# Kernel optimization log

Measured on AMD Instinct MI355X. Metric: run time of the kernel, lower is better.

The kernel has to match this reference:

```python
import jax, jax.numpy as jnp
import numpy as np

HID = 512; HH = HID // 2; INP = 1; OUT = 1
INH = int(HID * 0.3); EXC = HID - INH            # 153 / 359
N = 3 * HH + 2 * HID + INP                       # 1793 total units
ALM_EXC_START = 3 * HH + HID                      # start of ALM excitatory block
T_CONST = 0.1; SIGMA_REC = 0.01
B, T = 128, 300


def _np_masks():
    rng = np.random.default_rng(0)
    n_zeros = int(np.ceil(0.9 * HH))
    sparse = np.ones((HH, HH), np.float32)
    for c in range(HH):
        sparse[rng.permutation(HH)[:n_zeros], c] = 0.0
    alm2str = np.concatenate([np.ones((HH, EXC), np.float32), np.zeros((HH, INH), np.float32)], 1)
    thal2d1 = np.concatenate([np.ones((HH // 2, HID), np.float32), np.zeros((HH // 2, HID), np.float32)], 0)
    alm2d1 = 1.0 - thal2d1
    iti2d1 = np.concatenate([np.ones((HH // 2, INP), np.float32), np.zeros((HH // 2, INP), np.float32)], 0)
    alm_sign = np.concatenate([np.ones(EXC, np.float32), -np.ones(INH, np.float32)])  # alm2alm_D diagonal
    return sparse, alm2str, thal2d1, alm2d1, iti2d1, alm_sign

_SPARSE, _ALM2STR, _THAL2D1M, _ALM2D1M, _ITI2D1M, _ALMSIGN = [jnp.asarray(a) for a in _np_masks()]


def _clip(w):
    return jnp.clip(w, 1e-10, 1.0)               # F.hardtanh(w, 1e-10, 1)


def _build_W(d12d1_w, d12d2_w, d22d1_w, d22d2_w, d22stn_w, d12thal_w, stn2thal_w,
             thal2alm_w, alm2alm_w, thal2d1_w, thal2d2_w, alm2d1_w, alm2d2_w,
             inp_w_d1, inp_w_d2):
    z_ss = jnp.zeros((HH, HH)); z_sl = jnp.zeros((HH, HID))
    z_ls = jnp.zeros((HID, HH)); z_ll = jnp.zeros((HID, HID))
    z_si = jnp.zeros((HH, INP)); z_li = jnp.zeros((HID, INP))
    # striatal recurrence: sparse_mask * hardtanh(w) @ (-I)
    d12d1 = -(_SPARSE * _clip(d12d1_w)); d12d2 = -(_SPARSE * _clip(d12d2_w))
    d22d1 = -(_SPARSE * _clip(d22d1_w)); d22d2 = -(_SPARSE * _clip(d22d2_w))
    row_d1 = jnp.concatenate([d12d1, d22d1, z_ss, _THAL2D1M * _clip(thal2d1_w),
                              _ALM2D1M * _ALM2STR * _clip(alm2d1_w), _ITI2D1M * _clip(inp_w_d1)], 1)
    row_d2 = jnp.concatenate([d12d2, d22d2, z_ss, _clip(thal2d2_w),
                              _ALM2STR * _clip(alm2d2_w), _clip(inp_w_d2)], 1)
    row_stn = jnp.concatenate([z_ss, _clip(d22stn_w), z_ss, z_sl, z_sl, z_si], 1)
    row_thal = jnp.concatenate([_clip(d12thal_w), z_ls, -_clip(stn2thal_w), z_ll, z_ll, z_li], 1)  # stn2thal @ (-I)
    row_alm = jnp.concatenate([z_ls, z_ls, z_ls, _clip(thal2alm_w),
                               _clip(alm2alm_w) * _ALMSIGN[None, :], z_li], 1)      # alm2alm @ D (Dale)
    row_iti = jnp.zeros((INP, N))
    return jnp.concatenate([row_d1, row_d2, row_stn, row_thal, row_alm, row_iti], 0)


def setup_inputs() -> dict:
    key = jax.random.key(0)
    ks = jax.random.split(key, 24)
    u = lambda k, s: jax.random.uniform(k, s, jnp.float32) * 0.01   # uniform(0, 0.01) init
    return {
        "inp": jax.random.uniform(ks[0], (B, T, INP), jnp.float32),
        "cue_inp": jax.random.uniform(ks[1], (B, T, INP), jnp.float32),
        "inhib_stim": jnp.zeros((B, T, N), jnp.float32),
        "hn": jax.random.uniform(ks[2], (1, B, N), jnp.float32),
        "xn": jax.random.uniform(ks[3], (1, B, N), jnp.float32),
        "noise": jax.random.normal(ks[4], (B, T, N), jnp.float32),
        "d12d1_w": u(ks[5], (HH, HH)), "d12d2_w": u(ks[6], (HH, HH)),
        "d22d1_w": u(ks[7], (HH, HH)), "d22d2_w": u(ks[8], (HH, HH)),
        "d22stn_w": u(ks[9], (HH, HH)), "d12thal_w": u(ks[10], (HID, HH)),
        "stn2thal_w": u(ks[11], (HID, HH)), "thal2alm_w": u(ks[12], (HID, HID)),
        "alm2alm_w": u(ks[13], (HID, HID)), "thal2d1_w": u(ks[14], (HH, HID)),
        "thal2d2_w": u(ks[15], (HH, HID)), "alm2d1_w": u(ks[16], (HH, HID)),
        "alm2d2_w": u(ks[17], (HH, HID)), "inp_w_d1": u(ks[18], (HH, INP)),
        "inp_w_d2": u(ks[19], (HH, INP)), "out_w_alm": u(ks[20], (OUT, EXC)),
    }


def reference(inp, cue_inp, inhib_stim, hn, xn, noise,
              d12d1_w, d12d2_w, d22d1_w, d22d2_w, d22stn_w, d12thal_w, stn2thal_w,
              thal2alm_w, alm2alm_w, thal2d1_w, thal2d2_w, alm2d1_w, alm2d2_w,
              inp_w_d1, inp_w_d2, out_w_alm):
    W = _build_W(d12d1_w, d12d2_w, d22d1_w, d22d2_w, d22stn_w, d12thal_w, stn2thal_w,
                 thal2alm_w, alm2alm_w, thal2d1_w, thal2d2_w, alm2d1_w, alm2d2_w,
                 inp_w_d1, inp_w_d2)
    # tonic current: 0.1 everywhere except ITI units
    tonic = jnp.concatenate([0.1 * jnp.ones(N - INP, jnp.float32), jnp.zeros(INP, jnp.float32)])
    seq = (inhib_stim.swapaxes(0, 1),                 # [T, B, N]
           (inp + cue_inp).swapaxes(0, 1),            # [T, B, INP] -> injected into ITI units
           noise.swapaxes(0, 1))                      # [T, B, N]

    def step(carry, s):
        x, h = carry
        inh_t, iti_t, noise_t = s
        drive = h @ W.T + tonic + inh_t + SIGMA_REC * noise_t
        drive = drive.at[:, N - INP:].add(iti_t)
        x = x + T_CONST * (-x + drive)
        h = jax.nn.relu(x)
        out = h[:, ALM_EXC_START:ALM_EXC_START + EXC] @ out_w_alm.T
        return (x, h), (h, x, out)

    (_, _), (hs, xs, outs) = jax.lax.scan(step, (xn[0], hn[0]), seq)
    return hs.swapaxes(0, 1), xs.swapaxes(0, 1), outs.swapaxes(0, 1)
```

## Files before the change

kernel.cpp:

```cpp
#include <hip/hip_runtime.h>
#include <stdint.h>
#include <string.h>

#define NREAL 1793
#define NPAD  1824
#define NROWP 1808
#define WSTR  1832
#define NBLK  113
#define NGRP  2
#define TSTEPS 300
#define BATCH 128
#define XS_OFF 68851200
#define OUT_OFF 137702400
#define LOFF (16 * WSTR)
#define LOSCALE 4096.0f
#define LOINV  2.44140625e-4f

#define ARR_IDX(g,s)  (((g) * 8 + (s)) * 32)
#define MID_IDX(g)    ((16 + (g)) * 32)
#define FLAG_IDX(g,s) ((18 + (g) * 8 + (s)) * 32)
#define XLDR_IDX(g,x) ((40 + (g) * 8 + (x)) * 32)
#define XFLG_IDX(g,x) ((56 + (g) * 8 + (x)) * 32)
#define STRIPE_SZ(s)  ((s) == 0 ? 15u : 14u)

typedef _Float16 half_t;
typedef __attribute__((ext_vector_type(8))) _Float16 half8;
typedef __attribute__((ext_vector_type(4))) float f32x4;
typedef __attribute__((ext_vector_type(4))) unsigned int uint4v;

__device__ __forceinline__ float clipw(float w) {
  return fminf(fmaxf(w, 1e-10f), 1.0f);
}

__device__ __forceinline__ void store_pack_llc(uint32_t* p, uint32_t v) {
  asm volatile("global_store_dword %0, %1, off sc0 sc1"
               :: "v"((unsigned long long)(uintptr_t)p), "v"(v)
               : "memory");
}
__device__ __forceinline__ void store_f32_llc(float* p, float v) {
  asm volatile("global_store_dword %0, %1, off sc0 sc1"
               :: "v"((unsigned long long)(uintptr_t)p), "v"(v)
               : "memory");
}

__device__ __forceinline__ float unpack_h(uint32_t p) {
  unsigned short uh = (unsigned short)(p & 0xffffu);
  unsigned short ul = (unsigned short)(p >> 16);
  half_t hh = *(half_t*)&uh;
  half_t hl = *(half_t*)&ul;
  return (float)hh + LOINV * (float)hl;
}

template<int LO0, int N0, int LO1, int N1, int LO2, int N2>
__device__ __forceinline__ void seg_mfma(const uint32_t* __restrict__ ap,
                                         const half_t* __restrict__ Wl, int wl_b,
                                         f32x4& acc0, f32x4& acc1, f32x4& acc2)
{
  constexpr int NC = N0 + N1 + N2;
  if (NC == 0) return;
  uint4v q0[NC ? NC : 1], q1[NC ? NC : 1];
  #pragma unroll
  for (int i = 0; i < NC; ++i) {
    const int kc = (i < N0) ? (LO0 + i)
                 : (i < N0 + N1) ? (LO1 + i - N0)
                 : (LO2 + i - N0 - N1);
    q0[i] = *(const uint4v*)(ap + kc * 32);
    q1[i] = *(const uint4v*)(ap + kc * 32 + 4);
  }
  #pragma unroll
  for (int i = 0; i < NC; ++i) {
    const int kc = (i < N0) ? (LO0 + i)
                 : (i < N0 + N1) ? (LO1 + i - N0)
                 : (LO2 + i - N0 - N1);
    uint4v uh, ul;
    uh.x = __builtin_amdgcn_perm(q0[i].y, q0[i].x, 0x05040100u);
    uh.y = __builtin_amdgcn_perm(q0[i].w, q0[i].z, 0x05040100u);
    uh.z = __builtin_amdgcn_perm(q1[i].y, q1[i].x, 0x05040100u);
    uh.w = __builtin_amdgcn_perm(q1[i].w, q1[i].z, 0x05040100u);
    ul.x = __builtin_amdgcn_perm(q0[i].y, q0[i].x, 0x07060302u);
    ul.y = __builtin_amdgcn_perm(q0[i].w, q0[i].z, 0x07060302u);
    ul.z = __builtin_amdgcn_perm(q1[i].y, q1[i].x, 0x07060302u);
    ul.w = __builtin_amdgcn_perm(q1[i].w, q1[i].z, 0x07060302u);
    union { uint4v u; half8 h; } ch, cl;
    ch.u = uh; cl.u = ul;
    half8 bvh = *(const half8*)&Wl[wl_b + kc * 32];
    half8 bvl = *(const half8*)&Wl[LOFF + wl_b + kc * 32];
    acc0 = __builtin_amdgcn_mfma_f32_16x16x32_f16(ch.h, bvh, acc0, 0, 0, 0);
    acc1 = __builtin_amdgcn_mfma_f32_16x16x32_f16(ch.h, bvl, acc1, 0, 0, 0);
    acc2 = __builtin_amdgcn_mfma_f32_16x16x32_f16(cl.h, bvh, acc2, 0, 0, 0);
  }
}

__global__ __launch_bounds__(256)
void build_w(const float* __restrict__ d12d1, const float* __restrict__ d12d2,
             const float* __restrict__ d22d1, const float* __restrict__ d22d2,
             const float* __restrict__ d22stn, const float* __restrict__ d12thal,
             const float* __restrict__ stn2thal, const float* __restrict__ thal2alm,
             const float* __restrict__ alm2alm, const float* __restrict__ thal2d1,
             const float* __restrict__ thal2d2, const float* __restrict__ alm2d1,
             const float* __restrict__ alm2d2, const float* __restrict__ inpw1,
             const float* __restrict__ inpw2, const unsigned int* __restrict__ mbits,
             half_t* __restrict__ W)
{
  int idx = blockIdx.x * 256 + threadIdx.x;
  if (idx >= NROWP * NPAD) return;
  int i = idx / NPAD, j = idx - (idx / NPAD) * NPAD;
  float v = 0.f;
  if (i < NREAL && j < NREAL) {
    if (i < 256) {
      if (j < 512) {
        int jj = j & 255;
        unsigned bit = (mbits[(i << 3) + (jj >> 5)] >> (jj & 31)) & 1u;
        float wv = (j < 256) ? d12d1[(i << 8) + jj] : d22d1[(i << 8) + jj];
        v = bit ? -clipw(wv) : 0.f;
      } else if (j < 768) {
      } else if (j < 1280) {
        if (i < 128) v = clipw(thal2d1[(i << 9) + (j - 768)]);
      } else if (j < 1792) {
        int jj = j - 1280;
        if (i >= 128 && jj < 359) v = clipw(alm2d1[(i << 9) + jj]);
      } else {
        if (i < 128) v = clipw(inpw1[i]);
      }
    } else if (i < 512) {
      int ii = i - 256;
      if (j < 512) {
        int jj = j & 255;
        unsigned bit = (mbits[(ii << 3) + (jj >> 5)] >> (jj & 31)) & 1u;
        float wv = (j < 256) ? d12d2[(ii << 8) + jj] : d22d2[(ii << 8) + jj];
        v = bit ? -clipw(wv) : 0.f;
      } else if (j < 768) {
      } else if (j < 1280) {
        v = clipw(thal2d2[(ii << 9) + (j - 768)]);
      } else if (j < 1792) {
        int jj = j - 1280;
        if (jj < 359) v = clipw(alm2d2[(ii << 9) + jj]);
      } else {
        v = clipw(inpw2[ii]);
      }
    } else if (i < 768) {
      int ii = i - 512;
      if (j >= 256 && j < 512) v = clipw(d22stn[(ii << 8) + (j - 256)]);
    } else if (i < 1280) {
      int ii = i - 768;
      if (j < 256) v = clipw(d12thal[(ii << 8) + j]);
      else if (j >= 512 && j < 768) v = -clipw(stn2thal[(ii << 8) + (j - 512)]);
    } else if (i < 1792) {
      int ii = i - 1280;
      if (j >= 768 && j < 1280) v = clipw(thal2alm[(ii << 9) + (j - 768)]);
      else if (j >= 1280) {
        int jj = j - 1280;
        v = clipw(alm2alm[(ii << 9) + jj]) * ((jj < 359) ? 1.f : -1.f);
      }
    }
  }
  half_t vh = (half_t)v;
  half_t vl = (half_t)((v - (float)vh) * LOSCALE);
  W[idx] = vh;
  W[(size_t)NROWP * NPAD + idx] = vl;
}

__global__ __launch_bounds__(256)
void init_h(const float* __restrict__ hn, uint32_t* __restrict__ hbuf)
{
  const size_t P4 = (size_t)BATCH * NPAD;
  int idx = blockIdx.x * 256 + threadIdx.x;
  if (idx >= BATCH * NPAD) return;
  int b = idx / NPAD, k = idx - b * NPAD;
  float v = (k < NREAL) ? hn[b * NREAL + k] : 0.f;
  half_t vh = (half_t)v;
  half_t vl = (half_t)((v - (float)vh) * LOSCALE);
  uint32_t hp = (uint32_t)(*(unsigned short*)&vh) |
                ((uint32_t)(*(unsigned short*)&vl) << 16);
  hbuf[idx]      = hp;
  hbuf[P4 + idx] = 0u;
}

__global__ __launch_bounds__(256, 1)
void rnn_step_all(const half_t* __restrict__ Wg, uint32_t* __restrict__ hbuf,
                  unsigned int* __restrict__ cnt,
                  const float* __restrict__ inp, const float* __restrict__ cue,
                  const float* __restrict__ inhib, const float* __restrict__ noise,
                  const float* __restrict__ xn, const float* __restrict__ outw,
                  float* __restrict__ dout)
{
  __shared__ __align__(16) half_t Wl[2 * 16 * WSTR];
  const int tid = threadIdx.x;
  const int bid = blockIdx.x;
  const int g  = bid / NBLK;
  const int nb = bid - g * NBLK;
  const int r0 = nb * 16;
  const int bg = g * 64;
  const size_t P4 = (size_t)BATCH * NPAD;

  const int lane = tid & 63;
  const int w    = tid >> 6;
  const int n_i  = lane & 15;
  const int kq   = lane >> 4;
  const int row  = r0 + n_i;
  const bool valid = row < NREAL;
  const int b0 = bg + 16 * w + kq * 4;
  const int bA = bg + 16 * w + n_i;
  const int wl_b = n_i * WSTR + kq * 8;
  const bool is_outblk = (r0 == 512);
  const bool light = (r0 >= 512 && r0 < 1280) || (r0 == 1792);

  uint32_t xcc = 0;
  bool isldr = false;
  if (tid == 0) {
    asm volatile("s_getreg_b32 %0, hwreg(HW_REG_XCC_ID)" : "=s"(xcc));
    xcc &= 7u;
    if (light)
      isldr = (atomicCAS(&cnt[XLDR_IDX(g, xcc)], 0u, (uint32_t)bid + 1u) == 0u);
  }

  float inh[4], noi[4];
  #pragma unroll
  for (int r = 0; r < 4; ++r) {
    inh[r] = 0.f; noi[r] = 0.f;
    if (valid) {
      int ei = ((b0 + r) * TSTEPS) * NREAL + row;
      inh[r] = __builtin_nontemporal_load(&inhib[ei]);
      noi[r] = __builtin_nontemporal_load(&noise[ei]);
    }
  }

  for (int idx = tid; idx < 2 * 16 * (NPAD / 8); idx += 256) {
    int p   = idx / (16 * (NPAD / 8));
    int rem = idx - p * 16 * (NPAD / 8);
    int rr  = rem / (NPAD / 8);
    int cc  = (rem - rr * (NPAD / 8)) * 8;
    *(uint4v*)&Wl[p * LOFF + rr * WSTR + cc] =
        *(const uint4v*)&Wg[(size_t)p * NROWP * NPAD + (size_t)(r0 + rr) * NPAD + cc];
  }
  __syncthreads();

  if (tid == 0 && !light) {
    if (__hip_atomic_load(&cnt[XLDR_IDX(g, xcc)], __ATOMIC_RELAXED,
                          __HIP_MEMORY_SCOPE_AGENT) == 0u)
      isldr = (atomicCAS(&cnt[XLDR_IDX(g, xcc)], 0u, (uint32_t)bid + 1u) == 0u);
  }

  float xr[4];
  #pragma unroll
  for (int r = 0; r < 4; ++r)
    xr[r] = valid ? xn[(size_t)(b0 + r) * NREAL + row] : 0.f;

  const float tonic = (valid && row < 1792) ? 0.1f : 0.f;
  const bool is_iti = (row == 1792);

  const int ob    = bg + 16 * w + (lane >> 2);
  const int opart = lane & 3;
  const int ou0   = opart * 90;
  const int onu   = (opart == 3) ? 89 : 90;

  #pragma unroll 1
  for (int t = 0; t < TSTEPS; ++t) {
    const uint32_t* hr = hbuf + (size_t)(t & 1) * P4;
    uint32_t*       hw = hbuf + (size_t)((t & 1) ^ 1) * P4;

    float itv[4];
    #pragma unroll
    for (int r = 0; r < 4; ++r) {
      int bt = (b0 + r) * TSTEPS + t;
      itv[r] = is_iti ? (inp[bt] + cue[bt]) : 0.f;
    }

    const uint32_t* ap = hr + (size_t)bA * NPAD + kq * 8;
    f32x4 acc0 = {0.f, 0.f, 0.f, 0.f};
    f32x4 acc1 = {0.f, 0.f, 0.f, 0.f};
    f32x4 acc2 = {0.f, 0.f, 0.f, 0.f};

    if      (r0 < 128)  seg_mfma<0, 16, 24, 16, 56, 1>(ap, Wl, wl_b, acc0, acc1, acc2);
    else if (r0 < 256)  seg_mfma<0, 16, 40, 12,  0, 0>(ap, Wl, wl_b, acc0, acc1, acc2);
    else if (r0 < 512)  seg_mfma<0, 16, 24, 28, 56, 1>(ap, Wl, wl_b, acc0, acc1, acc2);
    else if (r0 < 768)  seg_mfma<8,  8,  0,  0,  0, 0>(ap, Wl, wl_b, acc0, acc1, acc2);
    else if (r0 < 1280) seg_mfma<0,  8, 16,  8,  0, 0>(ap, Wl, wl_b, acc0, acc1, acc2);
    else if (r0 < 1792) seg_mfma<24, 32, 0,  0,  0, 0>(ap, Wl, wl_b, acc0, acc1, acc2);

    #pragma unroll
    for (int r = 0; r < 4; ++r) {
      float drive = acc0[r] + LOINV * (acc1[r] + acc2[r])
                    + tonic + inh[r] + 0.01f * noi[r] + itv[r];
      float xv = xr[r] + 0.1f * (drive - xr[r]);
      float hv = fmaxf(xv, 0.f);
      xr[r] = xv;
      int bt = (b0 + r) * TSTEPS + t;
      if (valid) {
        int ei = bt * NREAL + row;
        store_f32_llc(&dout[ei], hv);
        store_f32_llc(&dout[XS_OFF + ei], xv);
      }
      half_t hh = (half_t)hv;
      half_t hl = (half_t)((hv - (float)hh) * LOSCALE);
      uint32_t hp = (uint32_t)(*(unsigned short*)&hh) |
                    ((uint32_t)(*(unsigned short*)&hl) << 16);
      store_pack_llc(&hw[(size_t)(b0 + r) * NPAD + row], hp);
    }

    if (is_outblk && t >= 1) {
      const uint32_t* hb = hr + (size_t)ob * NPAD + 1280 + ou0;
      float s = 0.f;
      #pragma unroll 10
      for (int i = 0; i < onu; ++i)
        s += unpack_h(hb[i]) * outw[ou0 + i];
      s += __shfl_xor(s, 1);
      s += __shfl_xor(s, 2);
      if (opart == 0)
        __builtin_nontemporal_store(s, &dout[OUT_OFF + ob * TSTEPS + (t - 1)]);
    }

    if (t + 1 < TSTEPS) {
      #pragma unroll
      for (int r = 0; r < 4; ++r) {
        if (valid) {
          int ei = ((b0 + r) * TSTEPS + (t + 1)) * NREAL + row;
          inh[r] = __builtin_nontemporal_load(&inhib[ei]);
          noi[r] = __builtin_nontemporal_load(&noise[ei]);
        }
      }
      asm volatile("s_waitcnt vmcnt(8)" ::: "memory");
      __builtin_amdgcn_s_barrier();
      if (tid == 0) {
        const int s = nb & 7;
        const unsigned epoch = (unsigned)(t + 1);
        unsigned old = atomicAdd(&cnt[ARR_IDX(g, s)], 1u);
        if (old == epoch * STRIPE_SZ(s) - 1u) {
          unsigned mo = atomicAdd(&cnt[MID_IDX(g)], 1u);
          if (mo == epoch * 8u - 1u) {
            #pragma unroll
            for (int f = 0; f < 8; ++f)
              __hip_atomic_store(&cnt[FLAG_IDX(g, f)], epoch,
                                 __ATOMIC_RELAXED, __HIP_MEMORY_SCOPE_AGENT);
          }
        }
        if (isldr) {
          int spins = 0;
          while (__hip_atomic_load(&cnt[FLAG_IDX(g, s)], __ATOMIC_RELAXED,
                                   __HIP_MEMORY_SCOPE_AGENT) < epoch) {
            if (spins < 4) { __builtin_amdgcn_s_sleep(1); }
            else           { __builtin_amdgcn_s_sleep(8); }
            ++spins;
          }
          __builtin_amdgcn_fence(__ATOMIC_ACQUIRE, "agent");
          asm volatile("s_waitcnt vmcnt(0)" ::: "memory");
          __hip_atomic_store(&cnt[XFLG_IDX(g, xcc)], epoch,
                             __ATOMIC_RELAXED, __HIP_MEMORY_SCOPE_AGENT);
        } else {
          int spins = 0;
          while (__hip_atomic_load(&cnt[XFLG_IDX(g, xcc)], __ATOMIC_RELAXED,
                                   __HIP_MEMORY_SCOPE_AGENT) < epoch) {
            if (spins < 4) { __builtin_amdgcn_s_sleep(1); }
            else           { __builtin_amdgcn_s_sleep(8); }
            ++spins;
          }
          asm volatile("buffer_inv sc0" ::: "memory");
        }
      }
      __builtin_amdgcn_s_barrier();
    }
  }

  asm volatile("s_waitcnt vmcnt(0)" ::: "memory");
  __builtin_amdgcn_s_barrier();
  if (tid == 0) {
    const int s = nb & 7;
    const unsigned epoch = (unsigned)TSTEPS;
    unsigned old = atomicAdd(&cnt[ARR_IDX(g, s)], 1u);
    if (old == epoch * STRIPE_SZ(s) - 1u) {
      unsigned mo = atomicAdd(&cnt[MID_IDX(g)], 1u);
      if (mo == epoch * 8u - 1u) {
        #pragma unroll
        for (int f = 0; f < 8; ++f)
          __hip_atomic_store(&cnt[FLAG_IDX(g, f)], epoch,
                             __ATOMIC_RELAXED, __HIP_MEMORY_SCOPE_AGENT);
      }
    }
  }
  if (is_outblk) {
    if (tid == 0) {
      const int s = nb & 7;
      int spins = 0;
      while (__hip_atomic_load(&cnt[FLAG_IDX(g, s)], __ATOMIC_RELAXED,
                               __HIP_MEMORY_SCOPE_AGENT) < (unsigned)TSTEPS) {
        if (spins < 4) { __builtin_amdgcn_s_sleep(1); }
        else           { __builtin_amdgcn_s_sleep(8); }
        ++spins;
      }
      __builtin_amdgcn_fence(__ATOMIC_ACQUIRE, "agent");
    }
    __builtin_amdgcn_s_barrier();
    const uint32_t* hr = hbuf + (size_t)(TSTEPS & 1) * P4;
    const uint32_t* hb = hr + (size_t)ob * NPAD + 1280 + ou0;
    float s = 0.f;
    #pragma unroll 10
    for (int i = 0; i < onu; ++i)
      s += unpack_h(hb[i]) * outw[ou0 + i];
    s += __shfl_xor(s, 1);
    s += __shfl_xor(s, 2);
    if (opart == 0)
      __builtin_nontemporal_store(s, &dout[OUT_OFF + ob * TSTEPS + (TSTEPS - 1)]);
  }
}

static void compute_sparse_mask(uint32_t* mb) {
  uint32_t pool[4];
  uint32_t hc = 0x43b0d7e5u;
  auto hashmix = [&hc](uint32_t value) -> uint32_t {
    value ^= hc; hc *= 0x931e8875u; value *= hc; value ^= value >> 16; return value;
  };
  auto mixf = [](uint32_t x, uint32_t y) -> uint32_t {
    uint32_t r = x * 0xca01f9ddu;
    r -= y * 0x4973f715u;
    r ^= r >> 16;
    return r;
  };
  for (int i = 0; i < 4; ++i) pool[i] = hashmix(0u);
  for (int s = 0; s < 4; ++s)
    for (int d = 0; d < 4; ++d)
      if (s != d) pool[d] = mixf(pool[d], hashmix(pool[s]));
  uint32_t st[8];
  uint32_t hb = 0x8b51f9ddu;
  for (int i = 0; i < 8; ++i) {
    uint32_t dv = pool[i & 3];
    dv ^= hb; hb *= 0x58f38dedu; dv *= hb; dv ^= dv >> 16;
    st[i] = dv;
  }
  uint64_t v64[4];
  for (int i = 0; i < 4; ++i) v64[i] = (uint64_t)st[2 * i] | ((uint64_t)st[2 * i + 1] << 32);
  typedef unsigned __int128 u128;
  const u128 MULT = ((u128)0x2360ed051fc65da4ULL << 64) | 0x4385df649fccf645ULL;
  u128 initstate = ((u128)v64[0] << 64) | v64[1];
  u128 initseq   = ((u128)v64[2] << 64) | v64[3];
  u128 state = 0, inc = (initseq << 1) | 1;
  state = state * MULT + inc;
  state += initstate;
  state = state * MULT + inc;
  bool has32 = false; uint32_t cached = 0;
  auto next64 = [&]() -> uint64_t {
    state = state * MULT + inc;
    uint64_t hi = (uint64_t)(state >> 64), lo = (uint64_t)state;
    unsigned rot = (unsigned)(state >> 122);
    uint64_t x = hi ^ lo;
    return (x >> rot) | (x << ((64 - rot) & 63));
  };
  auto next32 = [&]() -> uint32_t {
    if (has32) { has32 = false; return cached; }
    uint64_t v = next64();
    has32 = true; cached = (uint32_t)(v >> 32);
    return (uint32_t)v;
  };
  auto rinterval = [&](uint32_t mx) -> uint32_t {
    if (mx == 0) return 0;
    uint32_t mask = mx;
    mask |= mask >> 1; mask |= mask >> 2; mask |= mask >> 4;
    mask |= mask >> 8; mask |= mask >> 16;
    uint32_t value;
    do { value = next32() & mask; } while (value > mx);
    return value;
  };
  for (int i = 0; i < 256 * 8; ++i) mb[i] = 0xFFFFFFFFu;
  int perm[256];
  for (int c = 0; c < 256; ++c) {
    for (int i = 0; i < 256; ++i) perm[i] = i;
    for (int i = 255; i >= 1; --i) {
      uint32_t j = rinterval((uint32_t)i);
      int tmp = perm[i]; perm[i] = perm[j]; perm[j] = tmp;
    }
    for (int z = 0; z < 231; ++z)
      mb[perm[z] * 8 + (c >> 5)] &= ~(1u << (c & 31));
  }
}

extern "C" void kernel_launch(void* const* d_in, const int* in_sizes, int n_in,
                              void* d_out, int out_size, void* d_ws, size_t ws_size,
                              hipStream_t stream)
{
  (void)in_sizes; (void)n_in; (void)out_size; (void)ws_size;
  const float* inp   = (const float*)d_in[0];
  const float* cue   = (const float*)d_in[1];
  const float* inhib = (const float*)d_in[2];
  const float* hn    = (const float*)d_in[3];
  const float* xn    = (const float*)d_in[4];
  const float* noise = (const float*)d_in[5];
  const float* outw  = (const float*)d_in[21];
  float* dout = (float*)d_out;

  char* ws = (char*)d_ws;
  const size_t W_BYTES = (size_t)2 * NROWP * NPAD * sizeof(half_t);
  const size_t H_BYTES = (size_t)2 * BATCH * NPAD * 4;
  half_t*   W    = (half_t*)ws;
  uint32_t* hbuf = (uint32_t*)(ws + W_BYTES);
  unsigned int* mbits = (unsigned int*)(ws + W_BYTES + H_BYTES);
  unsigned int* cnt   = (unsigned int*)(ws + W_BYTES + H_BYTES + 16384);

  static uint32_t hmask[256 * 8];
  compute_sparse_mask(hmask);
  (void)hipMemcpyAsync(mbits, hmask, sizeof(hmask), hipMemcpyHostToDevice, stream);
  (void)hipMemsetAsync(cnt, 0, 16384, stream);

  build_w<<<(NROWP * NPAD + 255) / 256, 256, 0, stream>>>(
      (const float*)d_in[6],  (const float*)d_in[7],  (const float*)d_in[8],
      (const float*)d_in[9],  (const float*)d_in[10], (const float*)d_in[11],
      (const float*)d_in[12], (const float*)d_in[13], (const float*)d_in[14],
      (const float*)d_in[15], (const float*)d_in[16], (const float*)d_in[17],
      (const float*)d_in[18], (const float*)d_in[19], (const float*)d_in[20],
      mbits, W);
  init_h<<<(BATCH * NPAD + 255) / 256, 256, 0, stream>>>(hn, hbuf);

  void* args[] = {(void*)&W, (void*)&hbuf, (void*)&cnt, (void*)&inp, (void*)&cue,
                  (void*)&inhib, (void*)&noise, (void*)&xn, (void*)&outw, (void*)&dout};
  hipError_t err = hipLaunchCooperativeKernel(reinterpret_cast<void*>(rnn_step_all),
                                              dim3(NGRP * NBLK), dim3(256), args, 0, stream);
  if (err != hipSuccess) {
    rnn_step_all<<<dim3(NGRP * NBLK), dim3(256), 0, stream>>>(
        W, hbuf, cnt, inp, cue, inhib, noise, xn, outw, dout);
  }
}
```

Baseline: 4.133 ms.

## Replace hierarchical atomic-counter grid barrier with per-block epoch slots polled by leader waves

Each block now publishes its epoch to its own slot, and one full wave per XCC leader polls all 113 slots of its group, reducing them with a wave-wide min. This replaces the two-level atomicAdd counter tree (stripe counters, a mid counter, then flag fan-out). The aim is to drop the serialized atomic read-modify-write chain from the per-step grid barrier and cut its latency. The cost is heavier polling traffic from the leader waves. The final barrier is reworked the same way, so the output block now waits on its XCC flag.

```diff
diff --git a/kernel.cpp b/kernel.cpp
--- a/kernel.cpp
+++ b/kernel.cpp
@@ -16,12 +16,9 @@
 #define LOSCALE 4096.0f
 #define LOINV  2.44140625e-4f
 
-#define ARR_IDX(g,s)  (((g) * 8 + (s)) * 32)
-#define MID_IDX(g)    ((16 + (g)) * 32)
-#define FLAG_IDX(g,s) ((18 + (g) * 8 + (s)) * 32)
-#define XLDR_IDX(g,x) ((40 + (g) * 8 + (x)) * 32)
-#define XFLG_IDX(g,x) ((56 + (g) * 8 + (x)) * 32)
-#define STRIPE_SZ(s)  ((s) == 0 ? 15u : 14u)
+#define XLDR_IDX(g,x) (((g) * 8 + (x)) * 32)
+#define XFLG_IDX(g,x) ((16 + (g) * 8 + (x)) * 32)
+#define ASLOT(g,i)    (32 * 32 + (g) * 128 + (i))
 
 typedef _Float16 half_t;
 typedef __attribute__((ext_vector_type(8))) _Float16 half8;
@@ -32,7 +29,7 @@
   return fminf(fmaxf(w, 1e-10f), 1.0f);
 }
 
-__device__ __forceinline__ void store_pack_llc(uint32_t* p, uint32_t v) {
+__device__ __forceinline__ void store_u32_llc(unsigned int* p, unsigned int v) {
   asm volatile("global_store_dword %0, %1, off sc0 sc1"
                :: "v"((unsigned long long)(uintptr_t)p), "v"(v)
                : "memory");
@@ -185,6 +182,7 @@
                   float* __restrict__ dout)
 {
   __shared__ __align__(16) half_t Wl[2 * 16 * WSTR];
+  __shared__ unsigned int s_sync[2];
   const int tid = threadIdx.x;
   const int bid = blockIdx.x;
   const int g  = bid / NBLK;
@@ -206,12 +204,14 @@
   const bool light = (r0 >= 512 && r0 < 1280) || (r0 == 1792);
 
   uint32_t xcc = 0;
-  bool isldr = false;
   if (tid == 0) {
     asm volatile("s_getreg_b32 %0, hwreg(HW_REG_XCC_ID)" : "=s"(xcc));
     xcc &= 7u;
+    unsigned int ldr = 0;
     if (light)
-      isldr = (atomicCAS(&cnt[XLDR_IDX(g, xcc)], 0u, (uint32_t)bid + 1u) == 0u);
+      ldr = (atomicCAS(&cnt[XLDR_IDX(g, xcc)], 0u, (uint32_t)bid + 1u) == 0u);
+    s_sync[0] = xcc;
+    s_sync[1] = ldr;
   }
 
   float inh[4], noi[4];
@@ -236,10 +236,15 @@
   __syncthreads();
 
   if (tid == 0 && !light) {
-    if (__hip_atomic_load(&cnt[XLDR_IDX(g, xcc)], __ATOMIC_RELAXED,
+    if (__hip_atomic_load(&cnt[XLDR_IDX(g, s_sync[0])], __ATOMIC_RELAXED,
                           __HIP_MEMORY_SCOPE_AGENT) == 0u)
-      isldr = (atomicCAS(&cnt[XLDR_IDX(g, xcc)], 0u, (uint32_t)bid + 1u) == 0u);
-  }
+      s_sync[1] = (atomicCAS(&cnt[XLDR_IDX(g, s_sync[0])], 0u,
+                             (uint32_t)bid + 1u) == 0u);
+  }
+  __syncthreads();
+  const uint32_t xcc_b  = s_sync[0];
+  const bool     isldr  = (s_sync[1] != 0);
+  const bool lead_wave  = isldr && (tid < 64);
 
   float xr[4];
   #pragma unroll
@@ -295,7 +300,7 @@
       half_t hl = (half_t)((hv - (float)hh) * LOSCALE);
       uint32_t hp = (uint32_t)(*(unsigned short*)&hh) |
                     ((uint32_t)(*(unsigned short*)&hl) << 16);
-      store_pack_llc(&hw[(size_t)(b0 + r) * NPAD + row], hp);
+      store_u32_llc(&hw[(size_t)(b0 + r) * NPAD + row], hp);
     }
 
     if (is_outblk && t >= 1) {
@@ -319,43 +324,40 @@
           noi[r] = __builtin_nontemporal_load(&noise[ei]);
         }
       }
+      const unsigned epoch = (unsigned)(t + 1);
       asm volatile("s_waitcnt vmcnt(8)" ::: "memory");
       __builtin_amdgcn_s_barrier();
-      if (tid == 0) {
-        const int s = nb & 7;
-        const unsigned epoch = (unsigned)(t + 1);
-        unsigned old = atomicAdd(&cnt[ARR_IDX(g, s)], 1u);
-        if (old == epoch * STRIPE_SZ(s) - 1u) {
-          unsigned mo = atomicAdd(&cnt[MID_IDX(g)], 1u);
-          if (mo == epoch * 8u - 1u) {
-            #pragma unroll
-            for (int f = 0; f < 8; ++f)
-              __hip_atomic_store(&cnt[FLAG_IDX(g, f)], epoch,
-                                 __ATOMIC_RELAXED, __HIP_MEMORY_SCOPE_AGENT);
+      if (tid == 0)
+        store_u32_llc(&cnt[ASLOT(g, nb)], epoch);
+      if (lead_wave) {
+        unsigned m;
+        for (;;) {
+          unsigned v0 = __hip_atomic_load(&cnt[ASLOT(g, lane)],
+                                          __ATOMIC_RELAXED, __HIP_MEMORY_SCOPE_AGENT);
+          unsigned v1 = 0xFFFFFFFFu;
+          if (lane + 64 < NBLK)
+            v1 = __hip_atomic_load(&cnt[ASLOT(g, lane + 64)],
+                                   __ATOMIC_RELAXED, __HIP_MEMORY_SCOPE_AGENT);
+          m = v0 < v1 ? v0 : v1;
+          #pragma unroll
+          for (int o = 32; o; o >>= 1) {
+            unsigned mo = __shfl_xor(m, o);
+            m = m < mo ? m : mo;
           }
+          if (m >= epoch) break;
+          __builtin_amdgcn_s_sleep(2);
         }
-        if (isldr) {
-          int spins = 0;
-          while (__hip_atomic_load(&cnt[FLAG_IDX(g, s)], __ATOMIC_RELAXED,
-                                   __HIP_MEMORY_SCOPE_AGENT) < epoch) {
-            if (spins < 4) { __builtin_amdgcn_s_sleep(1); }
-            else           { __builtin_amdgcn_s_sleep(8); }
-            ++spins;
-          }
+        if (lane == 0) {
           __builtin_amdgcn_fence(__ATOMIC_ACQUIRE, "agent");
           asm volatile("s_waitcnt vmcnt(0)" ::: "memory");
-          __hip_atomic_store(&cnt[XFLG_IDX(g, xcc)], epoch,
+          __hip_atomic_store(&cnt[XFLG_IDX(g, xcc_b)], epoch,
                              __ATOMIC_RELAXED, __HIP_MEMORY_SCOPE_AGENT);
-        } else {
-          int spins = 0;
-          while (__hip_atomic_load(&cnt[XFLG_IDX(g, xcc)], __ATOMIC_RELAXED,
-                                   __HIP_MEMORY_SCOPE_AGENT) < epoch) {
-            if (spins < 4) { __builtin_amdgcn_s_sleep(1); }
-            else           { __builtin_amdgcn_s_sleep(8); }
-            ++spins;
-          }
-          asm volatile("buffer_inv sc0" ::: "memory");
         }
+      } else if (tid == 0) {
+        while (__hip_atomic_load(&cnt[XFLG_IDX(g, xcc_b)], __ATOMIC_RELAXED,
+                                 __HIP_MEMORY_SCOPE_AGENT) < epoch)
+          __builtin_amdgcn_s_sleep(2);
+        asm volatile("buffer_inv sc0" ::: "memory");
       }
       __builtin_amdgcn_s_barrier();
     }
@@ -363,32 +365,39 @@
 
   asm volatile("s_waitcnt vmcnt(0)" ::: "memory");
   __builtin_amdgcn_s_barrier();
-  if (tid == 0) {
-    const int s = nb & 7;
-    const unsigned epoch = (unsigned)TSTEPS;
-    unsigned old = atomicAdd(&cnt[ARR_IDX(g, s)], 1u);
-    if (old == epoch * STRIPE_SZ(s) - 1u) {
-      unsigned mo = atomicAdd(&cnt[MID_IDX(g)], 1u);
-      if (mo == epoch * 8u - 1u) {
-        #pragma unroll
-        for (int f = 0; f < 8; ++f)
-          __hip_atomic_store(&cnt[FLAG_IDX(g, f)], epoch,
-                             __ATOMIC_RELAXED, __HIP_MEMORY_SCOPE_AGENT);
-      }
-    }
+  if (tid == 0)
+    store_u32_llc(&cnt[ASLOT(g, nb)], (unsigned)TSTEPS);
+  if (lead_wave) {
+    unsigned m;
+    for (;;) {
+      unsigned v0 = __hip_atomic_load(&cnt[ASLOT(g, lane)],
+                                      __ATOMIC_RELAXED, __HIP_MEMORY_SCOPE_AGENT);
+      unsigned v1 = 0xFFFFFFFFu;
+      if (lane + 64 < NBLK)
+        v1 = __hip_atomic_load(&cnt[ASLOT(g, lane + 64)],
+                               __ATOMIC_RELAXED, __HIP_MEMORY_SCOPE_AGENT);
+      m = v0 < v1 ? v0 : v1;
+      #pragma unroll
+      for (int o = 32; o; o >>= 1) {
+        unsigned mo = __shfl_xor(m, o);
+        m = m < mo ? m : mo;
+      }
+      if (m >= (unsigned)TSTEPS) break;
+      __builtin_amdgcn_s_sleep(2);
+    }
+    if (lane == 0) {
+      __builtin_amdgcn_fence(__ATOMIC_ACQUIRE, "agent");
+      asm volatile("s_waitcnt vmcnt(0)" ::: "memory");
+      __hip_atomic_store(&cnt[XFLG_IDX(g, xcc_b)], (unsigned)TSTEPS,
+                         __ATOMIC_RELAXED, __HIP_MEMORY_SCOPE_AGENT);
+    }
+  } else if (is_outblk && tid == 0) {
+    while (__hip_atomic_load(&cnt[XFLG_IDX(g, xcc_b)], __ATOMIC_RELAXED,
+                             __HIP_MEMORY_SCOPE_AGENT) < (unsigned)TSTEPS)
+      __builtin_amdgcn_s_sleep(2);
+    asm volatile("buffer_inv sc0" ::: "memory");
   }
   if (is_outblk) {
-    if (tid == 0) {
-      const int s = nb & 7;
-      int spins = 0;
-      while (__hip_atomic_load(&cnt[FLAG_IDX(g, s)], __ATOMIC_RELAXED,
-                               __HIP_MEMORY_SCOPE_AGENT) < (unsigned)TSTEPS) {
-        if (spins < 4) { __builtin_amdgcn_s_sleep(1); }
-        else           { __builtin_amdgcn_s_sleep(8); }
-        ++spins;
-      }
-      __builtin_amdgcn_fence(__ATOMIC_ACQUIRE, "agent");
-    }
     __builtin_amdgcn_s_barrier();
     const uint32_t* hr = hbuf + (size_t)(TSTEPS & 1) * P4;
     const uint32_t* hb = hr + (size_t)ob * NPAD + 1280 + ou0;
```

Measured after the change: 4.196 ms. No clear change (+1.5%).
